# Kernel tuning notes

Hardware: AMD Instinct MI355X
Metric: run time of the kernel (lower is better)

The kernel has to match this reference:

```python
import jax, jax.numpy as jnp
import numpy as np

BLOCK = 64      # InformationEntropyAnalyzer block_size
BINS = 256      # InformationEntropyAnalyzer num_bins
EPS = 1e-12


def setup_inputs() -> dict:
    key = jax.random.key(0)
    x = jax.random.normal(key, (8, 64, 256, 256), dtype=jnp.float32)
    return {"x": x}


def _block_entropy(blocks):
    """Shannon entropy per block, matching np.histogram(density=True) math.

    blocks: (B, n) float32. Returns (B,) float32.
    """
    B, n = blocks.shape
    bmin = jnp.min(blocks, axis=1, keepdims=True)            # (B,1)
    bmax = jnp.max(blocks, axis=1, keepdims=True)            # (B,1)
    width = (bmax - bmin) / BINS                              # uniform bin width
    width_safe = jnp.where(width > 0, width, 1.0)
    # np.histogram: rightmost edge inclusive -> floor + clip reproduces it
    idx = jnp.clip(jnp.floor((blocks - bmin) / width_safe), 0, BINS - 1).astype(jnp.int32)
    row = jnp.arange(B, dtype=jnp.int32)[:, None]
    flat = (row * BINS + idx).reshape(-1)
    counts = jax.ops.segment_sum(
        jnp.ones((B * n,), jnp.float32), flat, num_segments=B * BINS
    ).reshape(B, BINS)
    density = counts / (n * width_safe)                       # density=True normalization
    p = density + EPS
    p = p / jnp.sum(p, axis=1, keepdims=True)
    return -jnp.sum(p * jnp.log2(p), axis=1)


def reference(x):
    """Faithful JAX version of InformationEntropyAnalyzer._compute_4d_entropy.

    Per (n,c) slice: split HxW into BLOCKxBLOCK tiles, compute Shannon entropy
    of the 256-bin histogram of each tile, then bilinearly upsample
    (align_corners=False, i.e. half-pixel, = jax.image.resize 'linear')
    back to (H, W).  Output: (N, C, H, W) entropy map.
    """
    N, C, H, W = x.shape
    nbh, nbw = H // BLOCK, W // BLOCK  # evenly divisible by construction
    blocks = (
        x.reshape(N, C, nbh, BLOCK, nbw, BLOCK)
        .transpose(0, 1, 2, 4, 3, 5)
        .reshape(N * C * nbh * nbw, BLOCK * BLOCK)
    )
    ent = _block_entropy(blocks).reshape(N, C, nbh, nbw)
    # F.interpolate(mode='bilinear', align_corners=False) == half-pixel linear resize
    return jax.image.resize(ent, (N, C, H, W), method='linear')
```

## Files before the change

### kernel.cpp

```cpp
#include <hip/hip_runtime.h>

#define NBINS 256
#define EPSF 1e-12f

typedef float v4f __attribute__((ext_vector_type(4)));

__global__ __launch_bounds__(256, 2) void fused_kernel(const float* __restrict__ x,
                                                       float* __restrict__ out) {
    const int nc   = blockIdx.x;
    const int t    = threadIdx.x;
    const int lane = t & 63;
    const int wave = t >> 6;

    __shared__ unsigned int hist[4][NBINS];
    __shared__ float ent_s[16];

    const float* cbase = x + ((size_t)nc << 16) + (size_t)wave * 64;
    unsigned int* h = hist[wave];

    v4f va[16], vb[16];

#define ISSUE(buf, s)                                                             \
    _Pragma("unroll")                                                             \
    for (int k = 0; k < 16; ++k) {                                                \
        const int f = lane + (k << 6);                    \
        buf[k] = *reinterpret_cast<const v4f*>(                                   \
            cbase + (size_t)(s) * (64 * 256) + (size_t)(f >> 4) * 256 + (f & 15) * 4); \
    }

#define PROCESS(buf, s)                                                           \
    {                                                                             \
        float lmin = INFINITY, lmax = -INFINITY;                                  \
        _Pragma("unroll")                                                         \
        for (int k = 0; k < 16; ++k) {                                            \
            lmin = fminf(lmin, fminf(fminf(buf[k].x, buf[k].y),                   \
                                     fminf(buf[k].z, buf[k].w)));                 \
            lmax = fmaxf(lmax, fmaxf(fmaxf(buf[k].x, buf[k].y),                   \
                                     fmaxf(buf[k].z, buf[k].w)));                 \
        }                                                                         \
        _Pragma("unroll")                                                         \
        for (int off = 32; off > 0; off >>= 1) {                                  \
            lmin = fminf(lmin, __shfl_xor(lmin, off));                            \
            lmax = fmaxf(lmax, __shfl_xor(lmax, off));                            \
        }                                                                         \
        uint4 z; z.x = z.y = z.z = z.w = 0u;       \
        reinterpret_cast<uint4*>(h)[lane] = z;                                    \
        const float width = (lmax - lmin) * (1.0f / NBINS);                       \
        const float wsafe = (width > 0.0f) ? width : 1.0f;                        \
        const float inv   = 1.0f / wsafe;                                         \
        const float coff  = -lmin * inv;                                          \
        _Pragma("unroll")                                                         \
        for (int k = 0; k < 16; ++k) {                                            \
            float vals[4] = {buf[k].x, buf[k].y, buf[k].z, buf[k].w};             \
            _Pragma("unroll")                                                     \
            for (int j = 0; j < 4; ++j) {                                         \
                      \
                int bin = (int)fmaf(vals[j], inv, coff);                          \
                bin = min(bin, 255);                                              \
                atomicAdd(&h[bin], 1u);                                           \
            }                                                                     \
        }                                                                         \
        const uint4 c    = reinterpret_cast<const uint4*>(h)[lane];               \
        const float pden = inv * (1.0f / 4096.0f);            \
        const float p0 = (float)c.x * pden + EPSF;                                \
        const float p1 = (float)c.y * pden + EPSF;                                \
        const float p2 = (float)c.z * pden + EPSF;                                \
        const float p3 = (float)c.w * pden + EPSF;                                \
        float s_ = p0 + p1 + p2 + p3;                                             \
        _Pragma("unroll")                                                         \
        for (int off = 32; off > 0; off >>= 1) s_ += __shfl_xor(s_, off);         \
        const float itot = 1.0f / s_;                                             \
        const float q0 = p0 * itot, q1 = p1 * itot;                               \
        const float q2 = p2 * itot, q3 = p3 * itot;                               \
        float e = q0 * log2f(q0) + q1 * log2f(q1)                                 \
                + q2 * log2f(q2) + q3 * log2f(q3);                                \
        _Pragma("unroll")                                                         \
        for (int off = 32; off > 0; off >>= 1) e += __shfl_xor(e, off);           \
        if (lane == 0) ent_s[((s) << 2) + wave] = -e;                             \
    }

    const int x4 = lane;
    const int ix = (int)floorf(((x4 << 2) + 0.5f) * 0.015625f - 0.5f);
    const int x0 = max(ix, 0), x1 = min(ix + 1, 3);
    v4f wv[4];
#pragma unroll
    for (int j = 0; j < 4; ++j) {
        const float fx = ((x4 << 2) + j + 0.5f) * 0.015625f - 0.5f;
        const float wx = fx - floorf(fx);
        const float a  = 1.0f - wx, bb = wx;
        wv[j].x = ((x0 == 0) ? a : 0.0f) + ((x1 == 0) ? bb : 0.0f);
        wv[j].y = ((x0 == 1) ? a : 0.0f) + ((x1 == 1) ? bb : 0.0f);
        wv[j].z = ((x0 == 2) ? a : 0.0f) + ((x1 == 2) ? bb : 0.0f);
        wv[j].w = ((x0 == 3) ? a : 0.0f) + ((x1 == 3) ? bb : 0.0f);
    }
    const v4f* er = reinterpret_cast<const v4f*>(ent_s);
    v4f* out4 = reinterpret_cast<v4f*>(out) + ((size_t)nc << 14);

#define WR(ystart, nrows)                                                         \
    _Pragma("unroll")                                                             \
    for (int i = 0; i < (nrows) / 4; ++i) {                                       \
        const int   y   = (ystart) + wave * ((nrows) / 4) + i;                    \
        const float fy  = (y + 0.5f) * 0.015625f - 0.5f;                          \
        const float fiy = floorf(fy);                                             \
        const float wy  = fy - fiy;                                               \
        const int   iy  = (int)fiy;                                               \
        const int   y0  = max(iy, 0), y1 = min(iy + 1, 3);                        \
        const v4f r0 = er[y0];                 \
        const v4f r1 = er[y1];                                                    \
        v4f rv = r0 * (1.0f - wy) + r1 * wy;                                      \
        v4f o;                                                                    \
        o.x = rv.x * wv[0].x + rv.y * wv[0].y + rv.z * wv[0].z + rv.w * wv[0].w;  \
        o.y = rv.x * wv[1].x + rv.y * wv[1].y + rv.z * wv[1].z + rv.w * wv[1].w;  \
        o.z = rv.x * wv[2].x + rv.y * wv[2].y + rv.z * wv[2].z + rv.w * wv[2].w;  \
        o.w = rv.x * wv[3].x + rv.y * wv[3].y + rv.z * wv[3].z + rv.w * wv[3].w;  \
        out4[(y << 6) + lane] = o;                                                \
    }

    ISSUE(va, 0)
    ISSUE(vb, 1)
    PROCESS(va, 0)
    ISSUE(va, 2)
    PROCESS(vb, 1)
    ISSUE(vb, 3)
    __syncthreads();
    WR(0, 96)
    PROCESS(va, 2)
    __syncthreads();
    WR(96, 64)
    PROCESS(vb, 3)
    __syncthreads();
    WR(160, 96)

#undef ISSUE
#undef PROCESS
#undef WR
}

extern "C" void kernel_launch(void* const* d_in, const int* in_sizes, int n_in,
                              void* d_out, int out_size, void* d_ws, size_t ws_size,
                              hipStream_t stream) {
    const float* x   = (const float*)d_in[0];
    float*       out = (float*)d_out;
    fused_kernel<<<512, 256, 0, stream>>>(x, out);
}
```

Baseline: 43.14 us.

## Process two (n,c) slices per block, prefetching the second slice during the first's tail

Each block now handles two consecutive (n,c) slices instead of one, and the grid is halved to 256 blocks. The loads for the second slice are issued while the first slice's last strips are processed and its output is written, so there is no pipeline bubble at the slice boundary. Separate entropy buffers keep the two slices' upsample inputs apart. In exchange, 256 blocks on an MI355X (256 CUs) gives only one block per CU, which lowers occupancy and the latency hiding that came from a second resident block.

Result: slower. 135.5 us (+214.2%).

```diff
diff --git a/kernel.cpp b/kernel.cpp
--- a/kernel.cpp
+++ b/kernel.cpp
@@ -7,28 +7,29 @@
 
 __global__ __launch_bounds__(256, 2) void fused_kernel(const float* __restrict__ x,
                                                        float* __restrict__ out) {
-    const int nc   = blockIdx.x;
+    const int bid  = blockIdx.x;
     const int t    = threadIdx.x;
     const int lane = t & 63;
     const int wave = t >> 6;
 
     __shared__ unsigned int hist[4][NBINS];
-    __shared__ float ent_s[16];
+    __shared__ float entA[16], entB[16];
 
-    const float* cbase = x + ((size_t)nc << 16) + (size_t)wave * 64;
+    const float* baseA = x + ((size_t)(2 * bid) << 16) + (size_t)wave * 64;
+    const float* baseB = baseA + (1 << 16);
     unsigned int* h = hist[wave];
 
     v4f va[16], vb[16];
 
-#define ISSUE(buf, s)                                                             \
+#define ISSUE(buf, base, s)                                                       \
     _Pragma("unroll")                                                             \
     for (int k = 0; k < 16; ++k) {                                                \
         const int f = lane + (k << 6);                    \
         buf[k] = *reinterpret_cast<const v4f*>(                                   \
-            cbase + (size_t)(s) * (64 * 256) + (size_t)(f >> 4) * 256 + (f & 15) * 4); \
+            (base) + (size_t)(s) * (64 * 256) + (size_t)(f >> 4) * 256 + (f & 15) * 4); \
     }
 
-#define PROCESS(buf, s)                                                           \
+#define PROCESS(buf, s, ent)                                                      \
     {                                                                             \
         float lmin = INFINITY, lmax = -INFINITY;                                  \
         _Pragma("unroll")                                                         \
@@ -76,7 +77,7 @@
                 + q2 * log2f(q2) + q3 * log2f(q3);                                \
         _Pragma("unroll")                                                         \
         for (int off = 32; off > 0; off >>= 1) e += __shfl_xor(e, off);           \
-        if (lane == 0) ent_s[((s) << 2) + wave] = -e;                             \
+        if (lane == 0) (ent)[((s) << 2) + wave] = -e;                             \
     }
 
     const int x4 = lane;
@@ -93,10 +94,10 @@
         wv[j].z = ((x0 == 2) ? a : 0.0f) + ((x1 == 2) ? bb : 0.0f);
         wv[j].w = ((x0 == 3) ? a : 0.0f) + ((x1 == 3) ? bb : 0.0f);
     }
-    const v4f* er = reinterpret_cast<const v4f*>(ent_s);
-    v4f* out4 = reinterpret_cast<v4f*>(out) + ((size_t)nc << 14);
+    v4f* outA4 = reinterpret_cast<v4f*>(out) + ((size_t)(2 * bid) << 14);
+    v4f* outB4 = outA4 + (1 << 14);
 
-#define WR(ystart, nrows)                                                         \
+#define WR(ent, out4, ystart, nrows)                                              \
     _Pragma("unroll")                                                             \
     for (int i = 0; i < (nrows) / 4; ++i) {                                       \
         const int   y   = (ystart) + wave * ((nrows) / 4) + i;                    \
@@ -105,31 +106,45 @@
         const float wy  = fy - fiy;                                               \
         const int   iy  = (int)fiy;                                               \
         const int   y0  = max(iy, 0), y1 = min(iy + 1, 3);                        \
-        const v4f r0 = er[y0];                 \
-        const v4f r1 = er[y1];                                                    \
+        const v4f r0 = reinterpret_cast<const v4f*>(ent)[y0];                     \
+        const v4f r1 = reinterpret_cast<const v4f*>(ent)[y1];                     \
         v4f rv = r0 * (1.0f - wy) + r1 * wy;                                      \
         v4f o;                                                                    \
         o.x = rv.x * wv[0].x + rv.y * wv[0].y + rv.z * wv[0].z + rv.w * wv[0].w;  \
         o.y = rv.x * wv[1].x + rv.y * wv[1].y + rv.z * wv[1].z + rv.w * wv[1].w;  \
         o.z = rv.x * wv[2].x + rv.y * wv[2].y + rv.z * wv[2].z + rv.w * wv[2].w;  \
         o.w = rv.x * wv[3].x + rv.y * wv[3].y + rv.z * wv[3].z + rv.w * wv[3].w;  \
-        out4[(y << 6) + lane] = o;                                                \
+        (out4)[(y << 6) + lane] = o;                                              \
     }
 
-    ISSUE(va, 0)
-    ISSUE(vb, 1)
-    PROCESS(va, 0)
-    ISSUE(va, 2)
-    PROCESS(vb, 1)
-    ISSUE(vb, 3)
+    ISSUE(va, baseA, 0)
+    ISSUE(vb, baseA, 1)
+    PROCESS(va, 0, entA)
+    ISSUE(va, baseA, 2)
+    PROCESS(vb, 1, entA)
+    ISSUE(vb, baseA, 3)
     __syncthreads();
-    WR(0, 96)
-    PROCESS(va, 2)
+    WR(entA, outA4, 0, 96)
+    PROCESS(va, 2, entA)
+    ISSUE(va, baseB, 0)
     __syncthreads();
-    WR(96, 64)
-    PROCESS(vb, 3)
+    WR(entA, outA4, 96, 64)
+    PROCESS(vb, 3, entA)
+    ISSUE(vb, baseB, 1)
     __syncthreads();
-    WR(160, 96)
+    WR(entA, outA4, 160, 96)
+    PROCESS(va, 0, entB)
+    ISSUE(va, baseB, 2)
+    PROCESS(vb, 1, entB)
+    ISSUE(vb, baseB, 3)
+    __syncthreads();
+    WR(entB, outB4, 0, 96)
+    PROCESS(va, 2, entB)
+    __syncthreads();
+    WR(entB, outB4, 96, 64)
+    PROCESS(vb, 3, entB)
+    __syncthreads();
+    WR(entB, outB4, 160, 96)
 
 #undef ISSUE
 #undef PROCESS
@@ -141,5 +156,5 @@
                               hipStream_t stream) {
     const float* x   = (const float*)d_in[0];
     float*       out = (float*)d_out;
-    fused_kernel<<<512, 256, 0, stream>>>(x, out);
+    fused_kernel<<<256, 256, 0, stream>>>(x, out);
 }
```
